# Optimization experiments

Hardware: AMD Instinct MI355X
Metric: run time of the kernel (lower is better)

## Reference

```python
import jax, jax.numpy as jnp
import numpy as np

ALPHA = 1.5
EPS = 1e-10


def quat_mul(a, b):
    # Hamilton product; last dim split into 4 quaternion components.
    aw, ax, ay, az = jnp.split(a, 4, axis=-1)
    bw, bx, by, bz = jnp.split(b, 4, axis=-1)
    w = aw * bw - ax * bx - ay * by - az * bz
    x = aw * bx + ax * bw + ay * bz - az * by
    y = aw * by - ax * bz + ay * bw + az * bx
    z = aw * bz + ax * by - ay * bx + az * bw
    return jnp.concatenate([w, x, y, z], axis=-1)


def setup_inputs() -> dict:
    key = jax.random.key(0)
    ks = jax.random.split(key, 8)
    B, S, D = 8, 2048, 1024  # D = embed_dim*4 with embed_dim=256
    scale = 1.0 / np.sqrt(D)
    return {
        "query": jax.random.normal(ks[0], (B, S, D), dtype=jnp.float32),
        "memory": jax.random.normal(ks[1], (B, S, D), dtype=jnp.float32),
        "wq": jax.random.normal(ks[2], (D, D), dtype=jnp.float32) * scale,
        "bq": jax.random.normal(ks[3], (D,), dtype=jnp.float32) * scale,
        "wk": jax.random.normal(ks[4], (D, D), dtype=jnp.float32) * scale,
        "bk": jax.random.normal(ks[5], (D,), dtype=jnp.float32) * scale,
        "wv": jax.random.normal(ks[6], (D, D), dtype=jnp.float32) * scale,
        "bv": jax.random.normal(ks[7], (D,), dtype=jnp.float32) * scale,
    }


def reference(query, memory, wq, bq, wk, bk, wv, bv):
    # Linear projections (nn.Linear equivalent)
    Q = query @ wq + bq        # [B, S, D]
    K = memory @ wk + bk       # [B, S, D] (memory_size must equal seq_len)
    V = memory @ wv + bv

    # FFT along sequence dim
    Qf = jnp.fft.fft(Q, axis=-2)
    Kf = jnp.fft.fft(K, axis=-2)
    Vf = jnp.fft.fft(V, axis=-2)

    # Spectral filter F(k) = exp(i * alpha * arctan(ln(|k| + eps)))
    S = Q.shape[-2]
    k = jnp.arange(S, dtype=jnp.float32)
    filt = jnp.exp(1j * ALPHA * jnp.arctan(jnp.log(k + EPS)))[:, None]  # [S, 1]

    Qf = Qf * filt
    Kf = Kf * filt
    Vf = Vf * filt

    # Quaternion Hamilton product chain (complex-valued)
    qkv = quat_mul(quat_mul(Qf, Kf), Vf)

    attended = jnp.fft.ifft(qkv, axis=-2).real
    return attended
```

## Files before the change

### kernel.cpp

```cpp
#include <hip/hip_runtime.h>

#define BB 8
#define SS 2048
#define DD 1024
#define EE 256
#define NFLOAT_T (BB * 2 * EE * 2 * SS)

typedef __attribute__((ext_vector_type(8))) short short8;
typedef __attribute__((ext_vector_type(4))) float f32x4;

__device__ __forceinline__ unsigned short f2bf(float x) {
  union { float f; unsigned u; } c; c.f = x;
  unsigned u = c.u + 0x7fffu + ((c.u >> 16) & 1u);
  return (unsigned short)(u >> 16);
}
__device__ __forceinline__ float bf2f(unsigned short h) {
  union { unsigned u; float f; } c; c.u = ((unsigned)h) << 16; return c.f;
}

__device__ __forceinline__ void gload_lds16(const void* g, void* l) {
  __builtin_amdgcn_global_load_lds((const __attribute__((address_space(1))) void*)g,
                                   (__attribute__((address_space(3))) void*)l, 16, 0, 0);
}

__device__ __forceinline__ float2 c_mul(float2 a, float2 b) {
  return make_float2(a.x * b.x - a.y * b.y, a.x * b.y + a.y * b.x);
}
__device__ __forceinline__ float2 c_add(float2 a, float2 b) { return make_float2(a.x + b.x, a.y + b.y); }
__device__ __forceinline__ float2 c_sub(float2 a, float2 b) { return make_float2(a.x - b.x, a.y - b.y); }

__device__ __forceinline__ void quat_mul_c(const float2* a, const float2* b, float2* r) {
  r[0] = c_sub(c_sub(c_sub(c_mul(a[0], b[0]), c_mul(a[1], b[1])), c_mul(a[2], b[2])), c_mul(a[3], b[3]));
  r[1] = c_sub(c_add(c_add(c_mul(a[0], b[1]), c_mul(a[1], b[0])), c_mul(a[2], b[3])), c_mul(a[3], b[2]));
  r[2] = c_add(c_add(c_sub(c_mul(a[0], b[2]), c_mul(a[1], b[3])), c_mul(a[2], b[0])), c_mul(a[3], b[1]));
  r[3] = c_add(c_sub(c_add(c_mul(a[0], b[3]), c_mul(a[1], b[2])), c_mul(a[2], b[1])), c_mul(a[3], b[0]));
}

__device__ __forceinline__ void unpack_pair(float2 zk, float2 zm,
                                            float2& Xk, float2& Yk, float2& Xm, float2& Ym) {
  Xk = make_float2(0.5f * (zk.x + zm.x), 0.5f * (zk.y - zm.y));
  Yk = make_float2(0.5f * (zk.y + zm.y), -0.5f * (zk.x - zm.x));
  Xm = make_float2(0.5f * (zm.x + zk.x), 0.5f * (zm.y - zk.y));
  Ym = make_float2(0.5f * (zm.y + zk.y), -0.5f * (zm.x - zk.x));
}

template <bool INV>
__device__ void fft2048_lds(float2* X, float2* Y, const float2* wtab, int tid) {
  float2* src = X;
  float2* dst = Y;
#pragma unroll
  for (int stage = 0; stage < 11; ++stage) {
    const int m = 1024 >> stage;
    const int sst = 1 << stage;
    for (int i = tid; i < 1024; i += 256) {
      const int p = i >> stage;
      const int q = i & (sst - 1);
      float2 a = src[q + sst * p];
      float2 b = src[q + sst * (p + m)];
      float2 w = wtab[p << stage];
      if (INV) w.y = -w.y;
      float2 amb = c_sub(a, b);
      dst[q + sst * (2 * p)] = c_add(a, b);
      dst[q + sst * (2 * p + 1)] = c_mul(amb, w);
    }
    __syncthreads();
    float2* t = src; src = dst; dst = t;
  }
}

__global__ __launch_bounds__(256) void convw_kernel(const float* __restrict__ W,
                                                    unsigned short* __restrict__ hiT,
                                                    unsigned short* __restrict__ loT) {
  __shared__ float t[32][33];
  const int tx = threadIdx.x & 31, ty = threadIdx.x >> 5;
  const int d0 = blockIdx.x * 32, k0 = blockIdx.y * 32;
#pragma unroll
  for (int r = 0; r < 4; ++r)
    t[ty + r * 8][tx] = W[(size_t)(k0 + ty + r * 8) * DD + d0 + tx];
  __syncthreads();
#pragma unroll
  for (int r = 0; r < 4; ++r) {
    float v = t[tx][ty + r * 8];
    unsigned short h = f2bf(v);
    hiT[(size_t)(d0 + ty + r * 8) * DD + k0 + tx] = h;
    loT[(size_t)(d0 + ty + r * 8) * DD + k0 + tx] = f2bf(v - bf2f(h));
  }
}

__global__ __launch_bounds__(256) void gemm_mfma_kernel(
    const float* __restrict__ A,
    const unsigned short* __restrict__ WThi, const unsigned short* __restrict__ WTlo,
    const float* __restrict__ bias, float* __restrict__ outp) {
  __shared__ char lds[65536];
  char* Wh = lds;
  char* Wl = lds + 16384;
  char* Ah = lds + 32768;
  char* Al = lds + 49152;

  const int tid = threadIdx.x;
  const int lane = tid & 63;
  const int w = tid >> 6;
  const int wr = w >> 1, wc = w & 1;
  const int b = blockIdx.z;
  const int d0 = blockIdx.y * 128;
  const int s0 = blockIdx.x * 128;

  const int lr = lane >> 3;
  const int sgslot = (lane & 7) ^ lr;

  const float* Ab = A + (size_t)b * SS * DD;

  f32x4 acc[4][4];
#pragma unroll
  for (int i = 0; i < 4; ++i)
#pragma unroll
    for (int j = 0; j < 4; ++j) acc[i][j] = (f32x4){0.f, 0.f, 0.f, 0.f};

  for (int k0 = 0; k0 < DD; k0 += 64) {
    const size_t kb = (size_t)k0 * 2 + (size_t)sgslot * 16;
#pragma unroll
    for (int j = 0; j < 4; ++j) {
      const int r = w * 32 + j * 8 + lr;
      const size_t wtoff = (size_t)(d0 + r) * 2048 + kb;
      const int loff = (w * 32 + j * 8) * 128;
      gload_lds16((const char*)WThi + wtoff, Wh + loff);
      gload_lds16((const char*)WTlo + wtoff, Wl + loff);
    }
#pragma unroll
    for (int j = 0; j < 4; ++j) {
      const int idx = j * 256 + tid;
      const int row = idx >> 3;
      const int slot = idx & 7;
      const float* src = Ab + (size_t)(s0 + row) * DD + k0 + slot * 8;
      float4 v0 = *(const float4*)(src);
      float4 v1 = *(const float4*)(src + 4);
      float va[8] = {v0.x, v0.y, v0.z, v0.w, v1.x, v1.y, v1.z, v1.w};
      union { short8 s8; unsigned short u[8]; } hu, lu;
#pragma unroll
      for (int e = 0; e < 8; ++e) {
        unsigned short h = f2bf(va[e]);
        hu.u[e] = h;
        lu.u[e] = f2bf(va[e] - bf2f(h));
      }
      const int off = row * 128 + (slot ^ (row & 7)) * 16;
      *(short8*)(Ah + off) = hu.s8;
      *(short8*)(Al + off) = lu.s8;
    }
    asm volatile("s_waitcnt vmcnt(0)" ::: "memory");
    __syncthreads();

    const int g = lane >> 4;
    const int m = lane & 15;
#pragma unroll
    for (int c = 0; c < 2; ++c) {
      short8 wa_h[4], wa_l[4], ab_h[4], ab_l[4];
#pragma unroll
      for (int i = 0; i < 4; ++i) {
        const int rowa = wr * 64 + i * 16 + m;
        const int offa = rowa * 128 + (((c << 2) + g) ^ (rowa & 7)) * 16;
        wa_h[i] = *(const short8*)(Wh + offa);
        wa_l[i] = *(const short8*)(Wl + offa);
        const int rowb = wc * 64 + i * 16 + m;
        const int offb = rowb * 128 + (((c << 2) + g) ^ (rowb & 7)) * 16;
        ab_h[i] = *(const short8*)(Ah + offb);
        ab_l[i] = *(const short8*)(Al + offb);
      }
#pragma unroll
      for (int i = 0; i < 4; ++i)
#pragma unroll
        for (int j = 0; j < 4; ++j) {
          acc[i][j] = __builtin_amdgcn_mfma_f32_16x16x32_bf16(wa_h[i], ab_h[j], acc[i][j], 0, 0, 0);
          acc[i][j] = __builtin_amdgcn_mfma_f32_16x16x32_bf16(wa_h[i], ab_l[j], acc[i][j], 0, 0, 0);
          acc[i][j] = __builtin_amdgcn_mfma_f32_16x16x32_bf16(wa_l[i], ab_h[j], acc[i][j], 0, 0, 0);
        }
    }
    __syncthreads();
  }

  const int g = lane >> 4, m = lane & 15;
#pragma unroll
  for (int i = 0; i < 4; ++i) {
#pragma unroll
    for (int r = 0; r < 4; ++r) {
      const int d = d0 + wr * 64 + i * 16 + g * 4 + r;
      const float bv = bias[d];
      const int p = (d >> 9) & 1, c2 = (d >> 8) & 1, e = d & 255;
      float* ob = outp + ((((size_t)b * 2 + p) * EE + e) * 2 + c2) * SS + s0 + wc * 64 + m;
#pragma unroll
      for (int j = 0; j < 4; ++j) ob[j * 16] = acc[i][j][r] + bv;
    }
  }
}

__global__ __launch_bounds__(256) void fft_fwd_kernel(float* __restrict__ ws) {
  __shared__ float2 bx[2048];
  __shared__ float2 by[2048];
  __shared__ float2 wt[1024];
  const int tid = threadIdx.x;
  const int e = blockIdx.x;
  const int p = blockIdx.y;
  const int z = blockIdx.z;
  const int t = z >> 3;
  const int b = z & 7;
  float* base = ws + (size_t)t * NFLOAT_T + ((((size_t)b * 2 + p) * EE + e) * 2) * SS;

  for (int j = tid; j < 1024; j += 256) {
    float sv, cv;
    sincosf(-6.283185307179586f * (float)j / 2048.0f, &sv, &cv);
    wt[j] = make_float2(cv, sv);
  }
  for (int s = tid; s < 2048; s += 256)
    bx[s] = make_float2(base[s], base[SS + s]);
  __syncthreads();

  fft2048_lds<false>(bx, by, wt, tid);

  float2* out2 = (float2*)base;
  for (int k = tid; k < 2048; k += 256) out2[k] = by[k];
}

__global__ __launch_bounds__(256) void quat_ifft_kernel(const float* __restrict__ ws,
                                                        float* __restrict__ out) {
  __shared__ float2 P0[2048];
  __shared__ float2 P1[2048];
  __shared__ float2 SC[2048];
  __shared__ float2 wt[1024];
  const int tid = threadIdx.x;
  const int e = blockIdx.x;
  const int b = blockIdx.y;

  const size_t cb0 = ((((size_t)b * 2 + 0) * EE + e) * 2) * SS;
  const size_t cb1 = ((((size_t)b * 2 + 1) * EE + e) * 2) * SS;
  const float2* Zq0 = (const float2*)(ws + cb0);
  const float2* Zq1 = (const float2*)(ws + cb1);
  const float2* Zk0 = (const float2*)(ws + (size_t)NFLOAT_T + cb0);
  const float2* Zk1 = (const float2*)(ws + (size_t)NFLOAT_T + cb1);
  const float2* Zv0 = (const float2*)(ws + 2 * (size_t)NFLOAT_T + cb0);
  const float2* Zv1 = (const float2*)(ws + 2 * (size_t)NFLOAT_T + cb1);

  for (int j = tid; j < 1024; j += 256) {
    float sv, cv;
    sincosf(-6.283185307179586f * (float)j / 2048.0f, &sv, &cv);
    wt[j] = make_float2(cv, sv);
  }

  for (int k = tid; k <= 1024; k += 256) {
    const int km = (2048 - k) & 2047;
    float2 Qk[4], Qm[4], Kk[4], Km[4], Vk[4], Vm[4];
    {
      float2 zk = Zq0[k], zm = Zq0[km];
      unpack_pair(zk, zm, Qk[0], Qk[1], Qm[0], Qm[1]);
      zk = Zq1[k]; zm = Zq1[km];
      unpack_pair(zk, zm, Qk[2], Qk[3], Qm[2], Qm[3]);
      zk = Zk0[k]; zm = Zk0[km];
      unpack_pair(zk, zm, Kk[0], Kk[1], Km[0], Km[1]);
      zk = Zk1[k]; zm = Zk1[km];
      unpack_pair(zk, zm, Kk[2], Kk[3], Km[2], Km[3]);
      zk = Zv0[k]; zm = Zv0[km];
      unpack_pair(zk, zm, Vk[0], Vk[1], Vm[0], Vm[1]);
      zk = Zv1[k]; zm = Zv1[km];
      unpack_pair(zk, zm, Vk[2], Vk[3], Vm[2], Vm[3]);
    }
    float2 t4[4], g1[4], g2[4];
    quat_mul_c(Qk, Kk, t4);
    quat_mul_c(t4, Vk, g1);
    quat_mul_c(Qm, Km, t4);
    quat_mul_c(t4, Vm, g2);

    float s3, c3;
    {
      const float th = 1.5f * atanf(logf((float)k + 1e-10f));
      sincosf(3.0f * th, &s3, &c3);
      const float2 f3 = make_float2(c3, s3);
#pragma unroll
      for (int c = 0; c < 4; ++c) g1[c] = c_mul(g1[c], f3);
    }
    {
      const float th = 1.5f * atanf(logf((float)km + 1e-10f));
      sincosf(3.0f * th, &s3, &c3);
      const float2 f3 = make_float2(c3, s3);
#pragma unroll
      for (int c = 0; c < 4; ++c) g2[c] = c_mul(g2[c], f3);
    }

    float2 Hk[4], Hm[4];
#pragma unroll
    for (int c = 0; c < 4; ++c) {
      Hk[c] = make_float2(0.5f * (g1[c].x + g2[c].x), 0.5f * (g1[c].y - g2[c].y));
      Hm[c] = make_float2(0.5f * (g2[c].x + g1[c].x), 0.5f * (g2[c].y - g1[c].y));
    }
    P0[k] = make_float2(Hk[0].x - Hk[1].y, Hk[0].y + Hk[1].x);
    P1[k] = make_float2(Hk[2].x - Hk[3].y, Hk[2].y + Hk[3].x);
    if (km != k) {
      P0[km] = make_float2(Hm[0].x - Hm[1].y, Hm[0].y + Hm[1].x);
      P1[km] = make_float2(Hm[2].x - Hm[3].y, Hm[2].y + Hm[3].x);
    }
  }
  __syncthreads();

  const float inv = 1.0f / 2048.0f;

  fft2048_lds<true>(P0, SC, wt, tid);
  for (int s = tid; s < 2048; s += 256) {
    float2 v = SC[s];
    out[((size_t)b * SS + s) * DD + 0 * EE + e] = v.x * inv;
    out[((size_t)b * SS + s) * DD + 1 * EE + e] = v.y * inv;
  }
  __syncthreads();

  fft2048_lds<true>(P1, SC, wt, tid);
  for (int s = tid; s < 2048; s += 256) {
    float2 v = SC[s];
    out[((size_t)b * SS + s) * DD + 2 * EE + e] = v.x * inv;
    out[((size_t)b * SS + s) * DD + 3 * EE + e] = v.y * inv;
  }
}

extern "C" void kernel_launch(void* const* d_in, const int* in_sizes, int n_in,
                              void* d_out, int out_size, void* d_ws, size_t ws_size,
                              hipStream_t stream) {
  const float* query = (const float*)d_in[0];
  const float* memory = (const float*)d_in[1];
  const float* wq = (const float*)d_in[2];
  const float* bq = (const float*)d_in[3];
  const float* wk = (const float*)d_in[4];
  const float* bk = (const float*)d_in[5];
  const float* wv = (const float*)d_in[6];
  const float* bv = (const float*)d_in[7];
  float* out = (float*)d_out;
  float* ws = (float*)d_ws;

  float* Qws = ws;
  float* Kws = ws + (size_t)NFLOAT_T;
  float* Vws = ws + 2 * (size_t)NFLOAT_T;

  unsigned short* Wq_hi = (unsigned short*)d_out;
  unsigned short* Wq_lo = Wq_hi + 1048576;
  unsigned short* Wk_hi = Wq_lo + 1048576;
  unsigned short* Wk_lo = Wk_hi + 1048576;
  unsigned short* Wv_hi = Wk_lo + 1048576;
  unsigned short* Wv_lo = Wv_hi + 1048576;

  convw_kernel<<<dim3(32, 32), 256, 0, stream>>>(wq, Wq_hi, Wq_lo);
  convw_kernel<<<dim3(32, 32), 256, 0, stream>>>(wk, Wk_hi, Wk_lo);
  convw_kernel<<<dim3(32, 32), 256, 0, stream>>>(wv, Wv_hi, Wv_lo);

  dim3 gg(SS / 128, DD / 128, BB);
  gemm_mfma_kernel<<<gg, 256, 0, stream>>>(query, Wq_hi, Wq_lo, bq, Qws);
  gemm_mfma_kernel<<<gg, 256, 0, stream>>>(memory, Wk_hi, Wk_lo, bk, Kws);
  gemm_mfma_kernel<<<gg, 256, 0, stream>>>(memory, Wv_hi, Wv_lo, bv, Vws);

  fft_fwd_kernel<<<dim3(EE, 2, 24), 256, 0, stream>>>(ws);

  quat_ifft_kernel<<<dim3(EE, BB), 256, 0, stream>>>(ws, out);
}
```

Before: 814.2 us.

## Stage inverse FFT output in workspace and add coalesced transpose kernel

The inverse-FFT kernel no longer writes each output element straight to the [B,S,D] tensor with a row stride of D floats. It now writes the contiguous float2 result back into the Q workspace region it has already consumed. A new tiled LDS transpose kernel then writes the output with coalesced float4 stores. Both FFT kernels also move from 256 to 512 threads per block, giving more parallel work per butterfly stage. The cost is an extra kernel launch plus one more read and write of the output-sized buffer.

After: 680.5 us. 1.2x faster.

```diff
diff --git a/kernel.cpp b/kernel.cpp
--- a/kernel.cpp
+++ b/kernel.cpp
@@ -44,7 +44,7 @@
   Ym = make_float2(0.5f * (zm.y + zk.y), -0.5f * (zm.x - zk.x));
 }
 
-template <bool INV>
+template <bool INV, int BLK>
 __device__ void fft2048_lds(float2* X, float2* Y, const float2* wtab, int tid) {
   float2* src = X;
   float2* dst = Y;
@@ -52,7 +52,7 @@
   for (int stage = 0; stage < 11; ++stage) {
     const int m = 1024 >> stage;
     const int sst = 1 << stage;
-    for (int i = tid; i < 1024; i += 256) {
+    for (int i = tid; i < 1024; i += BLK) {
       const int p = i >> stage;
       const int q = i & (sst - 1);
       float2 a = src[q + sst * p];
@@ -192,7 +192,7 @@
   }
 }
 
-__global__ __launch_bounds__(256) void fft_fwd_kernel(float* __restrict__ ws) {
+__global__ __launch_bounds__(512) void fft_fwd_kernel(float* __restrict__ ws) {
   __shared__ float2 bx[2048];
   __shared__ float2 by[2048];
   __shared__ float2 wt[1024];
@@ -204,23 +204,22 @@
   const int b = z & 7;
   float* base = ws + (size_t)t * NFLOAT_T + ((((size_t)b * 2 + p) * EE + e) * 2) * SS;
 
-  for (int j = tid; j < 1024; j += 256) {
+  for (int j = tid; j < 1024; j += 512) {
     float sv, cv;
     sincosf(-6.283185307179586f * (float)j / 2048.0f, &sv, &cv);
     wt[j] = make_float2(cv, sv);
   }
-  for (int s = tid; s < 2048; s += 256)
+  for (int s = tid; s < 2048; s += 512)
     bx[s] = make_float2(base[s], base[SS + s]);
   __syncthreads();
 
-  fft2048_lds<false>(bx, by, wt, tid);
+  fft2048_lds<false, 512>(bx, by, wt, tid);
 
   float2* out2 = (float2*)base;
-  for (int k = tid; k < 2048; k += 256) out2[k] = by[k];
-}
-
-__global__ __launch_bounds__(256) void quat_ifft_kernel(const float* __restrict__ ws,
-                                                        float* __restrict__ out) {
+  for (int k = tid; k < 2048; k += 512) out2[k] = by[k];
+}
+
+__global__ __launch_bounds__(512) void quat_ifft_kernel(float* __restrict__ ws) {
   __shared__ float2 P0[2048];
   __shared__ float2 P1[2048];
   __shared__ float2 SC[2048];
@@ -238,13 +237,13 @@
   const float2* Zv0 = (const float2*)(ws + 2 * (size_t)NFLOAT_T + cb0);
   const float2* Zv1 = (const float2*)(ws + 2 * (size_t)NFLOAT_T + cb1);
 
-  for (int j = tid; j < 1024; j += 256) {
+  for (int j = tid; j < 1024; j += 512) {
     float sv, cv;
     sincosf(-6.283185307179586f * (float)j / 2048.0f, &sv, &cv);
     wt[j] = make_float2(cv, sv);
   }
 
-  for (int k = tid; k <= 1024; k += 256) {
+  for (int k = tid; k <= 1024; k += 512) {
     const int km = (2048 - k) & 2047;
     float2 Qk[4], Qm[4], Kk[4], Km[4], Vk[4], Vm[4];
     {
@@ -300,19 +299,62 @@
 
   const float inv = 1.0f / 2048.0f;
 
-  fft2048_lds<true>(P0, SC, wt, tid);
-  for (int s = tid; s < 2048; s += 256) {
-    float2 v = SC[s];
-    out[((size_t)b * SS + s) * DD + 0 * EE + e] = v.x * inv;
-    out[((size_t)b * SS + s) * DD + 1 * EE + e] = v.y * inv;
+  fft2048_lds<true, 512>(P0, SC, wt, tid);
+  {
+    float2* oc = (float2*)(ws + cb0);
+    for (int s = tid; s < 2048; s += 512) {
+      float2 v = SC[s];
+      oc[s] = make_float2(v.x * inv, v.y * inv);
+    }
   }
   __syncthreads();
 
-  fft2048_lds<true>(P1, SC, wt, tid);
-  for (int s = tid; s < 2048; s += 256) {
-    float2 v = SC[s];
-    out[((size_t)b * SS + s) * DD + 2 * EE + e] = v.x * inv;
-    out[((size_t)b * SS + s) * DD + 3 * EE + e] = v.y * inv;
+  fft2048_lds<true, 512>(P1, SC, wt, tid);
+  {
+    float2* oc = (float2*)(ws + cb1);
+    for (int s = tid; s < 2048; s += 512) {
+      float2 v = SC[s];
+      oc[s] = make_float2(v.x * inv, v.y * inv);
+    }
+  }
+}
+
+#define TE 32
+#define TS 64
+__global__ __launch_bounds__(256) void transpose_out_kernel(const float* __restrict__ ws,
+                                                            float* __restrict__ out) {
+  __shared__ float L[4][TS][TE + 1];
+  const int tid = threadIdx.x;
+  const int b = blockIdx.z;
+  const int e0 = blockIdx.y * TE;
+  const int s0 = blockIdx.x * TS;
+
+  const int grp = tid >> 5;
+  const int l = tid & 31;
+#pragma unroll
+  for (int it = 0; it < 8; ++it) {
+    const int col = grp * 8 + it;
+    const int el = col >> 1;
+    const int p = col & 1;
+    const float2* cp = (const float2*)ws + (((size_t)b * 2 + p) * EE + (e0 + el)) * SS + s0;
+    float4 v = *(const float4*)(cp + 2 * l);
+    L[2 * p][2 * l][el] = v.x;
+    L[2 * p + 1][2 * l][el] = v.y;
+    L[2 * p][2 * l + 1][el] = v.z;
+    L[2 * p + 1][2 * l + 1][el] = v.w;
+  }
+  __syncthreads();
+
+#pragma unroll
+  for (int it = 0; it < 8; ++it) {
+    const int idx = it * 256 + tid;
+    const int c = idx >> 9;
+    const int rem = idx & 511;
+    const int s = rem >> 3;
+    const int f4 = rem & 7;
+    float4 v = make_float4(L[c][s][f4 * 4], L[c][s][f4 * 4 + 1],
+                           L[c][s][f4 * 4 + 2], L[c][s][f4 * 4 + 3]);
+    *(float4*)&out[((size_t)(b * SS + s0 + s)) * DD + c * EE + e0 + f4 * 4] = v;
   }
 }
 
@@ -350,7 +392,9 @@
   gemm_mfma_kernel<<<gg, 256, 0, stream>>>(memory, Wk_hi, Wk_lo, bk, Kws);
   gemm_mfma_kernel<<<gg, 256, 0, stream>>>(memory, Wv_hi, Wv_lo, bv, Vws);
 
-  fft_fwd_kernel<<<dim3(EE, 2, 24), 256, 0, stream>>>(ws);
-
-  quat_ifft_kernel<<<dim3(EE, BB), 256, 0, stream>>>(ws, out);
-}
+  fft_fwd_kernel<<<dim3(EE, 2, 24), 512, 0, stream>>>(ws);
+
+  quat_ifft_kernel<<<dim3(EE, BB), 512, 0, stream>>>(ws);
+
+  transpose_out_kernel<<<dim3(SS / TS, EE / TE, BB), 256, 0, stream>>>(ws, out);
+}
```
